# Optimization experiments

Hardware: AMD Instinct MI355X
Metric: run time of the kernel (lower is better)

## Reference

```python
import jax, jax.numpy as jnp
import numpy as np

D, K, N_NODES, E_DIM, H, L, HEADS, FF = 1024, 128, 200000, 384, 128, 2, 4, 128


def setup_inputs() -> dict:
    key = jax.random.key(0)
    ks = jax.random.split(key, 12)
    # regular graph: target node 0 has D neighbors (nodes 1..D); each neighbor n
    # has exactly K incoming edges, the first from tgt, the rest from random src != 0
    src = jax.random.randint(ks[0], (D, K), 1, N_NODES, dtype=jnp.int32)
    src = src.at[:, 0].set(0)
    dst = jnp.broadcast_to(jnp.arange(1, D + 1, dtype=jnp.int32)[:, None], (D, K))
    edge_index = jnp.stack([src.reshape(-1), dst.reshape(-1)])
    s = 0.05
    return {
        "tgt_x_index": jnp.zeros((1,), jnp.int32),
        "x": jax.random.normal(ks[1], (N_NODES, 64), jnp.float32),
        "edge_index": edge_index,
        "edge_attrs": jax.random.normal(ks[2], (D * K, E_DIM), jnp.float32),
        "first_token_marker": jax.random.normal(ks[3], (H,), jnp.float32),
        "proj_w": jax.random.normal(ks[4], (H, E_DIM), jnp.float32) * s,
        "proj_b": jnp.zeros((H,), jnp.float32),
        "attn_in_w": jax.random.normal(ks[5], (L, 3 * H, H), jnp.float32) * s,
        "attn_in_b": jnp.zeros((L, 3 * H), jnp.float32),
        "attn_out_w": jax.random.normal(ks[6], (L, H, H), jnp.float32) * s,
        "attn_out_b": jnp.zeros((L, H), jnp.float32),
        "ln1_g": jnp.ones((L, H), jnp.float32),
        "ln1_b": jnp.zeros((L, H), jnp.float32),
        "ff1_w": jax.random.normal(ks[7], (L, FF, H), jnp.float32) * s,
        "ff1_b": jnp.zeros((L, FF), jnp.float32),
        "ff2_w": jax.random.normal(ks[8], (L, H, FF), jnp.float32) * s,
        "ff2_b": jnp.zeros((L, H), jnp.float32),
        "ln2_g": jnp.ones((L, H), jnp.float32),
        "ln2_b": jnp.zeros((L, H), jnp.float32),
        "pred_w1": jax.random.normal(ks[9], (H, H), jnp.float32) * s,
        "pred_b1": jnp.zeros((H,), jnp.float32),
        "pred_w2": jax.random.normal(ks[10], (1, H), jnp.float32) * s,
        "pred_b2": jnp.zeros((1,), jnp.float32),
        "num_neighbors": D,
        "seq_len": K,
    }


def _ln(x, g, b):
    m = x.mean(-1, keepdims=True)
    v = ((x - m) ** 2).mean(-1, keepdims=True)
    return (x - m) * jax.lax.rsqrt(v + 1e-5) * g + b


def _forward(tgt_x_index, x, edge_index, edge_attrs, first_token_marker,
             proj_w, proj_b, attn_in_w, attn_in_b, attn_out_w, attn_out_b,
             ln1_g, ln1_b, ff1_w, ff1_b, ff2_w, ff2_b, ln2_g, ln2_b,
             pred_w1, pred_b1, pred_w2, pred_b2, num_neighbors, seq_len):
    tgt = tgt_x_index[0]
    src, dst = edge_index[0], edge_index[1]
    is_tgt = src == tgt
    # neighbors of target, in edge order (torch: edge_index[1][edge_index[0]==tgt])
    neigh_idx = jnp.nonzero(is_tgt, size=num_neighbors)[0]
    neigh_nodes = dst[neigh_idx]                       # [D]
    # fused ragged gather: map each edge to its neighbor slot, sort so that each
    # neighbor's edges are contiguous with the tgt->n edge first (stable sort
    # preserves original edge order within groups, matching boolean-mask gather)
    slot = jnp.full((x.shape[0],), num_neighbors, jnp.int32).at[neigh_nodes].set(
        jnp.arange(num_neighbors, dtype=jnp.int32))
    eslot = slot[dst]                                  # [E]
    sort_key = eslot.astype(jnp.int64) * 2 + jnp.where(is_tgt, 0, 1)
    order = jnp.argsort(sort_key)[: num_neighbors * seq_len]
    rows = edge_attrs[order].reshape(num_neighbors, seq_len, edge_attrs.shape[-1])
    hidden = proj_w.shape[0]
    hd = hidden // HEADS
    h = rows @ proj_w.T + proj_b                       # [D, K, H]
    h = h.at[:, 0, :].add(first_token_marker)          # first-token marker
    n_layers = attn_in_w.shape[0]
    for l in range(n_layers):
        qkv = h @ attn_in_w[l].T + attn_in_b[l]        # [D, K, 3H]
        q, k_, v = jnp.split(qkv, 3, axis=-1)
        q = q.reshape(num_neighbors, seq_len, HEADS, hd)
        k_ = k_.reshape(num_neighbors, seq_len, HEADS, hd)
        v = v.reshape(num_neighbors, seq_len, HEADS, hd)
        att = jax.nn.softmax(
            jnp.einsum('bqhd,bkhd->bhqk', q, k_) / jnp.sqrt(jnp.float32(hd)), axis=-1)
        o = jnp.einsum('bhqk,bkhd->bqhd', att, v).reshape(num_neighbors, seq_len, hidden)
        h = _ln(h + o @ attn_out_w[l].T + attn_out_b[l], ln1_g[l], ln1_b[l])
        f = jax.nn.relu(h @ ff1_w[l].T + ff1_b[l]) @ ff2_w[l].T + ff2_b[l]
        h = _ln(h + f, ln2_g[l], ln2_b[l])
    pooled = h.mean(axis=1)                            # mean over seq -> [D, H]
    final = pooled.mean(axis=0, keepdims=True)         # mean over neighbors -> [1, H]
    hmid = jax.nn.relu(final @ pred_w1.T + pred_b1)
    return jax.nn.sigmoid(hmid @ pred_w2.T + pred_b2)  # [1, 1]


def reference(tgt_x_index, x, edge_index, edge_attrs, first_token_marker,
              proj_w, proj_b, attn_in_w, attn_in_b, attn_out_w, attn_out_b,
              ln1_g, ln1_b, ff1_w, ff1_b, ff2_w, ff2_b, ln2_g, ln2_b,
              pred_w1, pred_b1, pred_w2, pred_b2, num_neighbors, seq_len):
    return _forward(tgt_x_index, x, edge_index, edge_attrs, first_token_marker,
                    proj_w, proj_b, attn_in_w, attn_in_b, attn_out_w, attn_out_b,
                    ln1_g, ln1_b, ff1_w, ff1_b, ff2_w, ff2_b, ln2_g, ln2_b,
                    pred_w1, pred_b1, pred_w2, pred_b2, num_neighbors, seq_len)
```

## Files before the change

### kernel.cpp

```cpp
#include <hip/hip_runtime.h>
#include <cstdint>
#include <cstddef>

#define D_N     1024
#define K_S     128
#define EDIM    384
#define HID     128
#define NHEAD   4
#define HDIM    32
#define FFD     128
#define NLAYER  2
#define ETOT    (D_N * K_S)
#define NNODES  200000
#define NBINS   (2 * D_N + 2)
#define NCH     1024
#define CHL     (ETOT / NCH)

#define OFF_ORDER 0u
#define OFF_KEY   0x080000u
#define OFF_SLOT  0x100000u
#define OFF_HIST  0x200000u
#define OFF_TOT   0xA02000u
#define OFF_WBF   0xA08000u
#define OFF_POOL  0xA80000u
#define WP_OFF 0
#define WI_OFF 49152
#define WO_OFF 147456
#define W1_OFF 180224
#define W2_OFF 212992
#define WTOT   245760

typedef __attribute__((ext_vector_type(8))) short  bf16x8;
typedef __attribute__((ext_vector_type(4))) short  short4v;
typedef __attribute__((ext_vector_type(4))) float  f32x4;

__device__ __forceinline__ short f2bf(float f) {
    union { float f; unsigned u; } v; v.f = f;
    unsigned r = v.u + 0x7fffu + ((v.u >> 16) & 1u);
    return (short)(r >> 16);
}
__device__ __forceinline__ int swz_off(int r, int byteInRow, int strideBytes) {
    return (r * strideBytes + byteInRow) ^ ((r & 7) << 4);
}

__global__ void init_cvt(int* __restrict__ slot, int* __restrict__ hist,
                         const float* __restrict__ p0, const float* __restrict__ p1,
                         const float* __restrict__ p2, const float* __restrict__ p3,
                         const float* __restrict__ p4, short* __restrict__ wbf)
{
    int idx = blockIdx.x * blockDim.x + threadIdx.x;
    int stride = gridDim.x * blockDim.x;
    for (int i = idx; i < NBINS * NCH; i += stride) hist[i] = 0;
    for (int i = idx; i < NNODES; i += stride) slot[i] = D_N;
    int i = idx * 8;
    if (i < WTOT) {
        const float* s;
        if      (i < WI_OFF) s = p0 + i;
        else if (i < WO_OFF) s = p1 + (i - WI_OFF);
        else if (i < W1_OFF) s = p2 + (i - WO_OFF);
        else if (i < W2_OFF) s = p3 + (i - W1_OFF);
        else                 s = p4 + (i - W2_OFF);
        float4 a = *(const float4*)s;
        float4 b = *(const float4*)(s + 4);
        bf16x8 o;
        o[0] = f2bf(a.x); o[1] = f2bf(a.y); o[2] = f2bf(a.z); o[3] = f2bf(a.w);
        o[4] = f2bf(b.x); o[5] = f2bf(b.y); o[6] = f2bf(b.z); o[7] = f2bf(b.w);
        *(bf16x8*)(wbf + i) = o;
    }
}

__global__ void find_neigh(const int* __restrict__ eidx,
                           const int* __restrict__ tgt_idx,
                           int* __restrict__ slot)
{
    __shared__ int wtot[16];
    __shared__ int wbase_s[16];
    __shared__ int neigh[D_N];
    const int tid  = threadIdx.x;
    const int lane = tid & 63;
    const int wv   = tid >> 6;
    const int tgt  = tgt_idx[0];
    const int* src = eidx;
    const int* dst = eidx + ETOT;
    const int epc  = ETOT / 1024;
    const int e0   = tid * epc;

    int c = 0;
    const int4* s4 = (const int4*)(src + e0);
    #pragma unroll 8
    for (int i = 0; i < epc / 4; ++i) {
        int4 v = s4[i];
        c += (v.x == tgt) + (v.y == tgt) + (v.z == tgt) + (v.w == tgt);
    }
    int incl = c;
    #pragma unroll
    for (int d = 1; d < 64; d <<= 1) {
        int t = __shfl_up(incl, d, 64);
        if (lane >= d) incl += t;
    }
    if (lane == 63) wtot[wv] = incl;
    __syncthreads();
    if (tid < 16) {
        int s = 0;
        for (int j = 0; j < tid; ++j) s += wtot[j];
        wbase_s[tid] = s;
    }
    __syncthreads();
    int r = wbase_s[wv] + incl - c;
    for (int e = e0; e < e0 + epc; ++e) {
        if (src[e] == tgt) { if (r < D_N) neigh[r] = dst[e]; ++r; }
    }
    __syncthreads();
    int total = wbase_s[15] + wtot[15];
    if (tid < total && tid < D_N) slot[neigh[tid]] = tid;
}

__global__ void compute_key(const int* __restrict__ eidx,
                            const int* __restrict__ tgt_idx,
                            const int* __restrict__ slot,
                            int* __restrict__ key)
{
    int e = blockIdx.x * 256 + threadIdx.x;
    if (e >= ETOT) return;
    int tgt = tgt_idx[0];
    key[e] = slot[eidx[ETOT + e]] * 2 + ((eidx[e] != tgt) ? 1 : 0);
}

__global__ void hist_build(const int* __restrict__ key, int* __restrict__ hist)
{
    const int c = blockIdx.x * 256 + threadIdx.x;
    if (c >= NCH) return;
    const int4* kp = (const int4*)(key + c * CHL);
    int cur = -1, run = 0;
    for (int i = 0; i < CHL / 4; ++i) {
        int4 k4 = kp[i];
        #pragma unroll
        for (int j = 0; j < 4; ++j) {
            int k = (j == 0) ? k4.x : (j == 1) ? k4.y : (j == 2) ? k4.z : k4.w;
            if (k == cur) { ++run; }
            else {
                if (run) hist[cur * NCH + c] += run;
                cur = k; run = 1;
            }
        }
    }
    if (run) hist[cur * NCH + c] += run;
}

__global__ void scan_pass1(const int* __restrict__ hist, int* __restrict__ tot)
{
    int b = blockIdx.x * 256 + threadIdx.x;
    if (b >= NBINS) return;
    const int4* h = (const int4*)(hist + b * NCH);
    int s = 0;
    #pragma unroll 4
    for (int c = 0; c < NCH / 4; ++c) { int4 v = h[c]; s += v.x + v.y + v.z + v.w; }
    tot[b] = s;
}

#define SCN 2176
__global__ void scan_pass2(int* __restrict__ tot)
{
    __shared__ int A[SCN];
    __shared__ int B[SCN];
    const int tid = threadIdx.x;
    for (int i = tid; i < SCN; i += 1024) A[i] = (i < NBINS) ? tot[i] : 0;
    __syncthreads();
    int* cur = A; int* nxt = B;
    for (int s = 1; s < SCN; s <<= 1) {
        for (int i = tid; i < SCN; i += 1024) nxt[i] = (i >= s) ? cur[i] + cur[i - s] : cur[i];
        __syncthreads();
        int* t = cur; cur = nxt; nxt = t;
    }
    for (int i = tid; i < NBINS; i += 1024) tot[i] = (i == 0) ? 0 : cur[i - 1];
}

__global__ void scan_pass3(int* __restrict__ hist, const int* __restrict__ base)
{
    const int wvg  = (blockIdx.x * blockDim.x + threadIdx.x) >> 6;
    const int lane = threadIdx.x & 63;
    if (wvg >= NBINS) return;
    int* h = hist + wvg * NCH + lane * 16;
    int4 a0 = ((int4*)h)[0], a1 = ((int4*)h)[1], a2 = ((int4*)h)[2], a3 = ((int4*)h)[3];
    int ls = a0.x + a0.y + a0.z + a0.w + a1.x + a1.y + a1.z + a1.w
           + a2.x + a2.y + a2.z + a2.w + a3.x + a3.y + a3.z + a3.w;
    int incl = ls;
    #pragma unroll
    for (int d = 1; d < 64; d <<= 1) {
        int t = __shfl_up(incl, d, 64);
        if (lane >= d) incl += t;
    }
    int run = base[wvg] + incl - ls;
    int4 o;
    o.x = run; run += a0.x; o.y = run; run += a0.y;
    o.z = run; run += a0.z; o.w = run; run += a0.w; ((int4*)h)[0] = o;
    o.x = run; run += a1.x; o.y = run; run += a1.y;
    o.z = run; run += a1.z; o.w = run; run += a1.w; ((int4*)h)[1] = o;
    o.x = run; run += a2.x; o.y = run; run += a2.y;
    o.z = run; run += a2.z; o.w = run; run += a2.w; ((int4*)h)[2] = o;
    o.x = run; run += a3.x; o.y = run; run += a3.y;
    o.z = run; run += a3.z; o.w = run; run += a3.w; ((int4*)h)[3] = o;
}

__global__ void scatter_order(const int* __restrict__ key,
                              int* __restrict__ hist,
                              int* __restrict__ order)
{
    const int c = blockIdx.x * 256 + threadIdx.x;
    if (c >= NCH) return;
    const int e0 = c * CHL;
    const int4* kp = (const int4*)(key + e0);
    int cur = -1, pos = 0;
    for (int i = 0; i < CHL / 4; ++i) {
        int4 k4 = kp[i];
        #pragma unroll
        for (int j = 0; j < 4; ++j) {
            int k = (j == 0) ? k4.x : (j == 1) ? k4.y : (j == 2) ? k4.z : k4.w;
            if (k != cur) {
                if (cur >= 0) hist[cur * NCH + c] = pos;
                cur = k;
                pos = hist[k * NCH + c];
            }
            if (pos >= 0 && pos < ETOT) order[pos] = e0 + i * 4 + j;
            ++pos;
        }
    }
    if (cur >= 0) hist[cur * NCH + c] = pos;
}

template<int CF, int KC, typename GetB>
__device__ __forceinline__ void gemm1(f32x4 (&acc)[CF],
    const char* aB, int aRow0, int aStride, int aColOff, int l15, int g, GetB getB)
{
    #pragma unroll
    for (int kc = 0; kc < KC; ++kc) {
        bf16x8 a = *(const bf16x8*)(aB +
            swz_off(aRow0 + l15, aColOff + kc * 64 + g * 16, aStride));
        #pragma unroll
        for (int cf = 0; cf < CF; ++cf)
            acc[cf] = __builtin_amdgcn_mfma_f32_16x16x32_bf16(a, getB(cf, kc), acc[cf], 0, 0, 0);
    }
}

template<int ROWB>
__device__ __forceinline__ void stage_w(const char* __restrict__ gsrc, char* ldst,
                                        int nbytes, int tid)
{
    #pragma unroll 4
    for (int u = tid * 16; u < nbytes; u += 512 * 16) {
        int row = u / ROWB;
        int in  = u - row * ROWB;
        *(bf16x8*)(ldst + swz_off(row, in, ROWB)) = *(const bf16x8*)(gsrc + u);
    }
}

template<int DROWB, int SROWB>
__device__ __forceinline__ void stage_sl(const char* __restrict__ gsrc, char* ldst,
                                         int nbytes, int tid)
{
    #pragma unroll 4
    for (int u = tid * 16; u < nbytes; u += 512 * 16) {
        int row = u / DROWB;
        int in  = u - row * DROWB;
        *(bf16x8*)(ldst + swz_off(row, in, DROWB)) =
            *(const bf16x8*)(gsrc + (size_t)row * SROWB + in);
    }
}

__device__ __forceinline__ void layer_norm1(f32x4 (&x)[8],
    const float* __restrict__ gg, const float* __restrict__ bb, int l15)
{
    float gv[8], bv[8];
    #pragma unroll
    for (int cf = 0; cf < 8; ++cf) { gv[cf] = gg[l15 + 16 * cf]; bv[cf] = bb[l15 + 16 * cf]; }
    #pragma unroll
    for (int rg = 0; rg < 4; ++rg) {
        float s = 0.f;
        #pragma unroll
        for (int cf = 0; cf < 8; ++cf) s += x[cf][rg];
        s += __shfl_xor(s, 1); s += __shfl_xor(s, 2);
        s += __shfl_xor(s, 4); s += __shfl_xor(s, 8);
        float mean = s * (1.f / 128.f);
        float v = 0.f;
        #pragma unroll
        for (int cf = 0; cf < 8; ++cf) { float d = x[cf][rg] - mean; v += d * d; }
        v += __shfl_xor(v, 1); v += __shfl_xor(v, 2);
        v += __shfl_xor(v, 4); v += __shfl_xor(v, 8);
        float rs = rsqrtf(v * (1.f / 128.f) + 1e-5f);
        #pragma unroll
        for (int cf = 0; cf < 8; ++cf)
            x[cf][rg] = (x[cf][rg] - mean) * rs * gv[cf] + bv[cf];
    }
}

__device__ __forceinline__ void write_hbf(const f32x4 (&x)[8], char* hbf_n,
                                          int l15, int g, int row0)
{
    #pragma unroll
    for (int cf = 0; cf < 8; ++cf)
        #pragma unroll
        for (int rg = 0; rg < 4; ++rg)
            *(short*)(hbf_n + swz_off(row0 + g * 4 + rg, (l15 + 16 * cf) * 2, 256)) =
                f2bf(x[cf][rg]);
}

__device__ __forceinline__ void attn_one(char* qb, const char* kb, const char* vb,
    const short* __restrict__ WOl, f32x4 (&hx)[8], int hd, int l15, int g, int row0)
{
    f32x4 sc[8];
    #pragma unroll
    for (int cf = 0; cf < 8; ++cf) sc[cf] = (f32x4){0.f, 0.f, 0.f, 0.f};
    gemm1<8, 1>(sc, qb, row0, 64, 0, l15, g,
        [&](int cf, int kc) {
            (void)kc;
            return *(const bf16x8*)(kb + swz_off(l15 + 16 * cf, g * 16, 64));
        });
    const float SC_ = 0.17677669529663687f;
    float inv_s[4];
    #pragma unroll
    for (int rg = 0; rg < 4; ++rg) {
        float mx = -1e30f;
        #pragma unroll
        for (int cf = 0; cf < 8; ++cf) {
            sc[cf][rg] *= SC_;
            mx = fmaxf(mx, sc[cf][rg]);
        }
        mx = fmaxf(mx, __shfl_xor(mx, 1)); mx = fmaxf(mx, __shfl_xor(mx, 2));
        mx = fmaxf(mx, __shfl_xor(mx, 4)); mx = fmaxf(mx, __shfl_xor(mx, 8));
        float sum = 0.f;
        #pragma unroll
        for (int cf = 0; cf < 8; ++cf) {
            float e = __expf(sc[cf][rg] - mx);
            sc[cf][rg] = e; sum += e;
        }
        sum += __shfl_xor(sum, 1); sum += __shfl_xor(sum, 2);
        sum += __shfl_xor(sum, 4); sum += __shfl_xor(sum, 8);
        inv_s[rg] = 1.f / sum;
    }
    f32x4 ov[2];
    ov[0] = (f32x4){0.f, 0.f, 0.f, 0.f};
    ov[1] = (f32x4){0.f, 0.f, 0.f, 0.f};
    #pragma unroll
    for (int cc = 0; cc < 4; ++cc) {
        #pragma unroll
        for (int q = 0; q < 2; ++q) {
            int cfi = 2 * cc + q;
            #pragma unroll
            for (int rg = 0; rg < 4; ++rg)
                *(short*)(qb + swz_off(row0 + g * 4 + rg, (l15 + 16 * q) * 2, 64)) =
                    f2bf(sc[cfi][rg] * inv_s[rg]);
        }
        gemm1<2, 1>(ov, qb, row0, 64, 0, l15, g,
            [&](int cf, int kc) {
                (void)kc;
                return *(const bf16x8*)(vb + swz_off(l15 + 16 * cf, cc * 64 + g * 16, 256));
            });
    }
    #pragma unroll
    for (int cf = 0; cf < 2; ++cf)
        #pragma unroll
        for (int rg = 0; rg < 4; ++rg)
            *(short*)(qb + swz_off(row0 + g * 4 + rg, (l15 + 16 * cf) * 2, 64)) =
                f2bf(ov[cf][rg]);
    gemm1<8, 1>(hx, qb, row0, 64, 0, l15, g,
        [&](int cf, int kc) {
            (void)kc;
            return *(const bf16x8*)(WOl +
                (size_t)(l15 + 16 * cf) * HID + hd * HDIM + g * 8);
        });
}

#define LDS_TOTAL 73728
__global__ __launch_bounds__(512, 2) void fused_mfma(
    const float* __restrict__ edge_attrs,
    const float* __restrict__ ftm,
    const short* __restrict__ wP, const float* __restrict__ projb,
    const short* __restrict__ wI, const float* __restrict__ aib,
    const short* __restrict__ wO, const float* __restrict__ aob,
    const float* __restrict__ l1g, const float* __restrict__ l1b,
    const short* __restrict__ w1, const float* __restrict__ f1b,
    const short* __restrict__ w2, const float* __restrict__ f2b,
    const float* __restrict__ l2g, const float* __restrict__ l2b,
    const int*   __restrict__ order,
    float*       __restrict__ pooled)
{
    __shared__ __align__(16) char sm[LDS_TOTAL];
    char* hbf  = sm;
    char* qkv  = sm + 32768;
    char* q_l  = qkv;
    char* k_l  = qkv + 8192;
    char* vT   = qkv + 16384;
    char* wb   = sm + 57344;
    char* wbB  = qkv + 8192;
    char* ebuf = qkv;
    char* fbuf = q_l;

    const int tid  = threadIdx.x;
    const int w    = tid >> 6;
    const int l    = tid & 63;
    const int l15  = l & 15;
    const int g    = l >> 4;
    const int row0 = 16 * w;
    const int b    = blockIdx.x;

    f32x4 hx[8];

    {
        #pragma unroll
        for (int cf = 0; cf < 8; ++cf) {
            float bs = projb[l15 + 16 * cf];
            hx[cf] = (f32x4){bs, bs, bs, bs};
        }
        const int prow = row0 + (l >> 2);
        const int rowIdx = order[b * K_S + prow];
        const float* arow = edge_attrs + (size_t)rowIdx * EDIM;
        const int doff = (l & 3) * 16;

        for (int ch = 0; ch < 6; ++ch) {
            stage_sl<128, 768>((const char*)wP + ch * 128, wb, 16384, tid);
            #pragma unroll
            for (int j = 0; j < 2; ++j) {
                float4 v0 = *(const float4*)(arow + ch * 64 + doff + j * 8);
                float4 v1 = *(const float4*)(arow + ch * 64 + doff + j * 8 + 4);
                bf16x8 pk;
                pk[0] = f2bf(v0.x); pk[1] = f2bf(v0.y); pk[2] = f2bf(v0.z); pk[3] = f2bf(v0.w);
                pk[4] = f2bf(v1.x); pk[5] = f2bf(v1.y); pk[6] = f2bf(v1.z); pk[7] = f2bf(v1.w);
                *(bf16x8*)(ebuf + swz_off(prow, (doff + j * 8) * 2, 128)) = pk;
            }
            __syncthreads();
            gemm1<8, 2>(hx, ebuf, row0, 128, 0, l15, g,
                [&](int cf, int kc) {
                    return *(const bf16x8*)(wb + swz_off(l15 + 16 * cf, kc * 64 + g * 16, 128));
                });
            __syncthreads();
        }
        if (w == 0 && g == 0) {
            #pragma unroll
            for (int cf = 0; cf < 8; ++cf) hx[cf][0] += ftm[l15 + 16 * cf];
        }
        write_hbf(hx, hbf, l15, g, row0);
        stage_w<256>((const char*)wI, wb, 8192, tid);
        stage_w<256>((const char*)(wI + (size_t)HID * HID), wb + 8192, 8192, tid);
        __syncthreads();
    }

    for (int ly = 0; ly < NLAYER; ++ly) {
        const short* WIl = wI + (size_t)ly * 3 * HID * HID;
        const float* bI  = aib + ly * 3 * HID;
        const short* WOl = wO + (size_t)ly * HID * HID;
        const float* bO  = aob + ly * HID;
        const short* W1l = w1 + (size_t)ly * FFD * HID;
        const float* b1  = f1b + ly * FFD;
        const short* W2l = w2 + (size_t)ly * HID * FFD;
        const float* b2v = f2b + ly * HID;

        #pragma unroll
        for (int cf = 0; cf < 8; ++cf) {
            float bs = bO[l15 + 16 * cf];
            #pragma unroll
            for (int rg = 0; rg < 4; ++rg) hx[cf][rg] += bs;
        }

        for (int hd = 0; hd < NHEAD; ++hd) {
            f32x4 acc[6];
            #pragma unroll
            for (int cf = 0; cf < 6; ++cf) {
                float bs = bI[(cf >> 1) * HID + hd * HDIM + l15 + 16 * (cf & 1)];
                acc[cf] = (f32x4){bs, bs, bs, bs};
            }
            gemm1<6, 4>(acc, hbf, row0, 256, 0, l15, g,
                [&](int cf, int kc) {
                    if (cf < 2)
                        return *(const bf16x8*)(wb +
                            swz_off(l15 + 16 * cf, kc * 64 + g * 16, 256));
                    else if (cf < 4)
                        return *(const bf16x8*)(wb + 8192 +
                            swz_off(l15 + 16 * (cf - 2), kc * 64 + g * 16, 256));
                    else
                        return *(const bf16x8*)(WIl +
                            (size_t)(2 * HID + hd * HDIM + l15 + 16 * (cf - 4)) * HID +
                            kc * 32 + g * 8);
                });
            #pragma unroll
            for (int cf = 0; cf < 2; ++cf) {
                int dcol = (l15 + 16 * cf) * 2;
                #pragma unroll
                for (int rg = 0; rg < 4; ++rg) {
                    int row = row0 + g * 4 + rg;
                    *(short*)(q_l + swz_off(row, dcol, 64)) = f2bf(acc[cf][rg]);
                    *(short*)(k_l + swz_off(row, dcol, 64)) = f2bf(acc[2 + cf][rg]);
                }
                short4v pv;
                pv[0] = f2bf(acc[4 + cf][0]); pv[1] = f2bf(acc[4 + cf][1]);
                pv[2] = f2bf(acc[4 + cf][2]); pv[3] = f2bf(acc[4 + cf][3]);
                *(short4v*)(vT + swz_off(l15 + 16 * cf, (row0 + g * 4) * 2, 256)) = pv;
            }
            __syncthreads();

            if (hd < NHEAD - 1) {
                stage_w<256>((const char*)(WIl + (size_t)((hd + 1) * HDIM) * HID),
                             wb, 8192, tid);
                stage_w<256>((const char*)(WIl + (size_t)(HID + (hd + 1) * HDIM) * HID),
                             wb + 8192, 8192, tid);
            } else {
                stage_w<256>((const char*)W1l, wb, 8192, tid);
                stage_sl<64, 256>((const char*)W2l, wb + 8192, 8192, tid);
            }
            attn_one(q_l, k_l, vT, WOl, hx, hd, l15, g, row0);
            __syncthreads();
        }

        layer_norm1(hx, l1g + ly * HID, l1b + ly * HID, l15);
        write_hbf(hx, hbf, l15, g, row0);

        f32x4 yy[8];
        #pragma unroll
        for (int cf = 0; cf < 8; ++cf) {
            float bs = b2v[l15 + 16 * cf];
            yy[cf] = (f32x4){bs, bs, bs, bs};
        }
        #pragma unroll
        for (int qq = 0; qq < 4; ++qq) {
            char* bw = (qq & 1) ? wbB : wb;
            f32x4 fq[2];
            #pragma unroll
            for (int cf = 0; cf < 2; ++cf) {
                float bs = b1[qq * 32 + l15 + 16 * cf];
                fq[cf] = (f32x4){bs, bs, bs, bs};
            }
            gemm1<2, 4>(fq, hbf, row0, 256, 0, l15, g,
                [&](int cf, int kc) {
                    return *(const bf16x8*)(bw + swz_off(l15 + 16 * cf, kc * 64 + g * 16, 256));
                });
            if (qq < 3) {
                char* nb = (qq & 1) ? wb : wbB;
                stage_w<256>((const char*)(W1l + (size_t)((qq + 1) * 32) * HID),
                             nb, 8192, tid);
                stage_sl<64, 256>((const char*)W2l + (qq + 1) * 64, nb + 8192, 8192, tid);
            } else if (ly + 1 < NLAYER) {
                const short* WIn = wI + (size_t)(ly + 1) * 3 * HID * HID;
                stage_w<256>((const char*)WIn, wb, 8192, tid);
                stage_w<256>((const char*)(WIn + (size_t)HID * HID), wb + 8192, 8192, tid);
            }
            #pragma unroll
            for (int cf = 0; cf < 2; ++cf)
                #pragma unroll
                for (int rg = 0; rg < 4; ++rg)
                    *(short*)(fbuf + swz_off(row0 + g * 4 + rg, (l15 + 16 * cf) * 2, 64)) =
                        f2bf(fmaxf(fq[cf][rg], 0.f));
            gemm1<8, 1>(yy, fbuf, row0, 64, 0, l15, g,
                [&](int cf, int kc) {
                    (void)kc;
                    return *(const bf16x8*)(bw + 8192 + swz_off(l15 + 16 * cf, g * 16, 64));
                });
            __syncthreads();
        }
        #pragma unroll
        for (int cf = 0; cf < 8; ++cf) yy[cf] += hx[cf];
        layer_norm1(yy, l2g + ly * HID, l2b + ly * HID, l15);
        #pragma unroll
        for (int cf = 0; cf < 8; ++cf) hx[cf] = yy[cf];
        write_hbf(hx, hbf, l15, g, row0);
    }

    float* pool_s = (float*)qkv;
    #pragma unroll
    for (int cf = 0; cf < 8; ++cf) {
        float s = hx[cf][0] + hx[cf][1] + hx[cf][2] + hx[cf][3];
        s += __shfl_xor(s, 16); s += __shfl_xor(s, 32);
        if (g == 0) pool_s[w * 128 + l15 + 16 * cf] = s;
    }
    __syncthreads();
    if (tid < 128) {
        float s = 0.f;
        #pragma unroll
        for (int ww = 0; ww < 8; ++ww) s += pool_s[ww * 128 + tid];
        pooled[b * HID + tid] = s * (1.f / 128.f);
    }
}

__global__ void final_pred(const float* __restrict__ pooled,
                           const float* __restrict__ w1, const float* __restrict__ b1,
                           const float* __restrict__ w2, const float* __restrict__ b2,
                           float* __restrict__ out)
{
    __shared__ float part[4][HID];
    __shared__ float fin[HID];
    __shared__ float hm[HID];
    const int tid = threadIdx.x;
    const int f = tid & 127, q = tid >> 7;
    float s = 0.f;
    for (int bb = q * 256; bb < (q + 1) * 256; ++bb) s += pooled[bb * HID + f];
    part[q][f] = s;
    __syncthreads();
    if (tid < HID) {
        fin[tid] = (part[0][tid] + part[1][tid] + part[2][tid] + part[3][tid])
                   * (1.f / (float)D_N);
    }
    __syncthreads();
    if (tid < HID) {
        float a = b1[tid];
        for (int k = 0; k < HID; ++k) a += fin[k] * w1[tid * HID + k];
        hm[tid] = fmaxf(a, 0.f) * w2[tid];
    }
    __syncthreads();
    if (tid == 0) {
        float z = 0.f;
        for (int j = 0; j < HID; ++j) z += hm[j];
        z += b2[0];
        out[0] = 1.f / (1.f + __expf(-z));
    }
}

extern "C" void kernel_launch(void* const* d_in, const int* in_sizes, int n_in,
                              void* d_out, int out_size, void* d_ws, size_t ws_size,
                              hipStream_t stream)
{
    (void)in_sizes; (void)n_in; (void)out_size; (void)ws_size;

    const int*   tgt   = (const int*)  d_in[0];
    const int*   eidx  = (const int*)  d_in[2];
    const float* eattr = (const float*)d_in[3];
    const float* ftm   = (const float*)d_in[4];
    const float* projw = (const float*)d_in[5];
    const float* projb = (const float*)d_in[6];
    const float* aiw   = (const float*)d_in[7];
    const float* aib   = (const float*)d_in[8];
    const float* aow   = (const float*)d_in[9];
    const float* aob   = (const float*)d_in[10];
    const float* l1g   = (const float*)d_in[11];
    const float* l1b   = (const float*)d_in[12];
    const float* f1w   = (const float*)d_in[13];
    const float* f1b   = (const float*)d_in[14];
    const float* f2w   = (const float*)d_in[15];
    const float* f2b   = (const float*)d_in[16];
    const float* l2g   = (const float*)d_in[17];
    const float* l2b   = (const float*)d_in[18];
    const float* pw1   = (const float*)d_in[19];
    const float* pb1   = (const float*)d_in[20];
    const float* pw2   = (const float*)d_in[21];
    const float* pb2   = (const float*)d_in[22];

    char* ws = (char*)d_ws;
    int*   order  = (int*)  (ws + OFF_ORDER);
    int*   key    = (int*)  (ws + OFF_KEY);
    int*   slot   = (int*)  (ws + OFF_SLOT);
    int*   hist   = (int*)  (ws + OFF_HIST);
    int*   tot    = (int*)  (ws + OFF_TOT);
    float* pooled = (float*)(ws + OFF_POOL);
    short* wbf    = (short*)(ws + OFF_WBF);

    init_cvt     <<<dim3(2048), dim3(256),  0, stream>>>(slot, hist,
                                                         projw, aiw, aow, f1w, f2w, wbf);
    find_neigh   <<<dim3(1),    dim3(1024), 0, stream>>>(eidx, tgt, slot);
    compute_key  <<<dim3(512),  dim3(256),  0, stream>>>(eidx, tgt, slot, key);
    hist_build   <<<dim3(4),    dim3(256),  0, stream>>>(key, hist);
    scan_pass1   <<<dim3(9),    dim3(256),  0, stream>>>(hist, tot);
    scan_pass2   <<<dim3(1),    dim3(1024), 0, stream>>>(tot);
    scan_pass3   <<<dim3(513),  dim3(256),  0, stream>>>(hist, tot);
    scatter_order<<<dim3(4),    dim3(256),  0, stream>>>(key, hist, order);

    fused_mfma<<<dim3(D_N), dim3(512), 0, stream>>>(
        eattr, ftm,
        wbf + WP_OFF, projb,
        wbf + WI_OFF, aib,
        wbf + WO_OFF, aob,
        l1g, l1b,
        wbf + W1_OFF, f1b,
        wbf + W2_OFF, f2b,
        l2g, l2b,
        order, pooled);

    final_pred<<<dim3(1), dim3(512), 0, stream>>>(pooled, pw1, pb1, pw2, pb2, (float*)d_out);
}
```

Baseline: 511.5 us.

## Process two neighbor sequences per 1024-thread block sharing staged weights with double buffering

Each block now handles two neighbor sequences with 1024 threads, so weight tiles staged into LDS are shared by both sequences and staged half as often per sequence. The projection and QKV weight staging uses two ping-pong buffers so the next chunk loads while the current one is consumed, and the V weights come from LDS instead of global memory. In exchange LDS use grows to 160KB per block, which allows only one block per CU, and each barrier now spans 16 waves.

After: 566.4 us. 10.7% more time.

```diff
diff --git a/kernel.cpp b/kernel.cpp
--- a/kernel.cpp
+++ b/kernel.cpp
@@ -246,8 +246,8 @@
 __device__ __forceinline__ void stage_w(const char* __restrict__ gsrc, char* ldst,
                                         int nbytes, int tid)
 {
-    #pragma unroll 4
-    for (int u = tid * 16; u < nbytes; u += 512 * 16) {
+    #pragma unroll 2
+    for (int u = tid * 16; u < nbytes; u += 1024 * 16) {
         int row = u / ROWB;
         int in  = u - row * ROWB;
         *(bf16x8*)(ldst + swz_off(row, in, ROWB)) = *(const bf16x8*)(gsrc + u);
@@ -258,8 +258,8 @@
 __device__ __forceinline__ void stage_sl(const char* __restrict__ gsrc, char* ldst,
                                          int nbytes, int tid)
 {
-    #pragma unroll 4
-    for (int u = tid * 16; u < nbytes; u += 512 * 16) {
+    #pragma unroll 2
+    for (int u = tid * 16; u < nbytes; u += 1024 * 16) {
         int row = u / DROWB;
         int in  = u - row * DROWB;
         *(bf16x8*)(ldst + swz_off(row, in, DROWB)) =
@@ -370,8 +370,8 @@
         });
 }
 
-#define LDS_TOTAL 73728
-__global__ __launch_bounds__(512, 2) void fused_mfma(
+#define LDS_TOTAL 163840
+__global__ __launch_bounds__(1024) void fused_mfma(
     const float* __restrict__ edge_attrs,
     const float* __restrict__ ftm,
     const short* __restrict__ wP, const float* __restrict__ projb,
@@ -385,23 +385,23 @@
     float*       __restrict__ pooled)
 {
     __shared__ __align__(16) char sm[LDS_TOTAL];
-    char* hbf  = sm;
-    char* qkv  = sm + 32768;
-    char* q_l  = qkv;
-    char* k_l  = qkv + 8192;
-    char* vT   = qkv + 16384;
-    char* wb   = sm + 57344;
-    char* wbB  = qkv + 8192;
-    char* ebuf = qkv;
+    const int tid = threadIdx.x;
+    const int w   = tid >> 6;
+    const int nb  = w >> 3;
+    const int l   = tid & 63;
+    const int l15 = l & 15;
+    const int g   = l >> 4;
+    const int row0 = (w & 7) * 16;
+    const int b   = blockIdx.x;
+
+    char* hbf  = sm + nb * 32768;
+    char* q_l  = sm + 65536 + nb * 16384;
+    char* k_l  = q_l + 8192;
+    char* vT   = sm + 98304 + nb * 8192;
+    char* ebuf = q_l;
     char* fbuf = q_l;
-
-    const int tid  = threadIdx.x;
-    const int w    = tid >> 6;
-    const int l    = tid & 63;
-    const int l15  = l & 15;
-    const int g    = l >> 4;
-    const int row0 = 16 * w;
-    const int b    = blockIdx.x;
+    char* wb0  = sm + 114688;
+    char* wb1  = sm + 139264;
 
     f32x4 hx[8];
 
@@ -412,12 +412,15 @@
             hx[cf] = (f32x4){bs, bs, bs, bs};
         }
         const int prow = row0 + (l >> 2);
-        const int rowIdx = order[b * K_S + prow];
+        const int rowIdx = order[(2 * b + nb) * K_S + prow];
         const float* arow = edge_attrs + (size_t)rowIdx * EDIM;
         const int doff = (l & 3) * 16;
 
+        stage_sl<128, 768>((const char*)wP, wb0, 16384, tid);
+        __syncthreads();
+
         for (int ch = 0; ch < 6; ++ch) {
-            stage_sl<128, 768>((const char*)wP + ch * 128, wb, 16384, tid);
+            char* cw = (ch & 1) ? wb1 : wb0;
             #pragma unroll
             for (int j = 0; j < 2; ++j) {
                 float4 v0 = *(const float4*)(arow + ch * 64 + doff + j * 8);
@@ -427,21 +430,26 @@
                 pk[4] = f2bf(v1.x); pk[5] = f2bf(v1.y); pk[6] = f2bf(v1.z); pk[7] = f2bf(v1.w);
                 *(bf16x8*)(ebuf + swz_off(prow, (doff + j * 8) * 2, 128)) = pk;
             }
+            if (ch < 5) {
+                stage_sl<128, 768>((const char*)wP + (ch + 1) * 128,
+                                   (ch & 1) ? wb0 : wb1, 16384, tid);
+            } else {
+                stage_w<256>((const char*)wI, wb0, 8192, tid);
+                stage_w<256>((const char*)(wI + (size_t)HID * HID), wb0 + 8192, 8192, tid);
+                stage_w<256>((const char*)(wI + (size_t)(2 * HID) * HID), wb0 + 16384, 8192, tid);
+            }
             __syncthreads();
             gemm1<8, 2>(hx, ebuf, row0, 128, 0, l15, g,
                 [&](int cf, int kc) {
-                    return *(const bf16x8*)(wb + swz_off(l15 + 16 * cf, kc * 64 + g * 16, 128));
+                    return *(const bf16x8*)(cw + swz_off(l15 + 16 * cf, kc * 64 + g * 16, 128));
                 });
             __syncthreads();
         }
-        if (w == 0 && g == 0) {
+        if ((w & 7) == 0 && g == 0) {
             #pragma unroll
             for (int cf = 0; cf < 8; ++cf) hx[cf][0] += ftm[l15 + 16 * cf];
         }
         write_hbf(hx, hbf, l15, g, row0);
-        stage_w<256>((const char*)wI, wb, 8192, tid);
-        stage_w<256>((const char*)(wI + (size_t)HID * HID), wb + 8192, 8192, tid);
-        __syncthreads();
     }
 
     for (int ly = 0; ly < NLAYER; ++ly) {
@@ -462,6 +470,7 @@
         }
 
         for (int hd = 0; hd < NHEAD; ++hd) {
+            char* cw = (hd & 1) ? wb1 : wb0;
             f32x4 acc[6];
             #pragma unroll
             for (int cf = 0; cf < 6; ++cf) {
@@ -470,16 +479,8 @@
             }
             gemm1<6, 4>(acc, hbf, row0, 256, 0, l15, g,
                 [&](int cf, int kc) {
-                    if (cf < 2)
-                        return *(const bf16x8*)(wb +
-                            swz_off(l15 + 16 * cf, kc * 64 + g * 16, 256));
-                    else if (cf < 4)
-                        return *(const bf16x8*)(wb + 8192 +
-                            swz_off(l15 + 16 * (cf - 2), kc * 64 + g * 16, 256));
-                    else
-                        return *(const bf16x8*)(WIl +
-                            (size_t)(2 * HID + hd * HDIM + l15 + 16 * (cf - 4)) * HID +
-                            kc * 32 + g * 8);
+                    return *(const bf16x8*)(cw + (cf >> 1) * 8192 +
+                        swz_off(l15 + 16 * (cf & 1), kc * 64 + g * 16, 256));
                 });
             #pragma unroll
             for (int cf = 0; cf < 2; ++cf) {
@@ -497,14 +498,17 @@
             }
             __syncthreads();
 
+            char* nw = (hd & 1) ? wb0 : wb1;
             if (hd < NHEAD - 1) {
                 stage_w<256>((const char*)(WIl + (size_t)((hd + 1) * HDIM) * HID),
-                             wb, 8192, tid);
+                             nw, 8192, tid);
                 stage_w<256>((const char*)(WIl + (size_t)(HID + (hd + 1) * HDIM) * HID),
-                             wb + 8192, 8192, tid);
+                             nw + 8192, 8192, tid);
+                stage_w<256>((const char*)(WIl + (size_t)(2 * HID + (hd + 1) * HDIM) * HID),
+                             nw + 16384, 8192, tid);
             } else {
-                stage_w<256>((const char*)W1l, wb, 8192, tid);
-                stage_sl<64, 256>((const char*)W2l, wb + 8192, 8192, tid);
+                stage_w<256>((const char*)W1l, nw, 8192, tid);
+                stage_sl<64, 256>((const char*)W2l, nw + 8192, 8192, tid);
             }
             attn_one(q_l, k_l, vT, WOl, hx, hd, l15, g, row0);
             __syncthreads();
@@ -521,7 +525,7 @@
         }
         #pragma unroll
         for (int qq = 0; qq < 4; ++qq) {
-            char* bw = (qq & 1) ? wbB : wb;
+            char* bw = (qq & 1) ? wb1 : wb0;
             f32x4 fq[2];
             #pragma unroll
             for (int cf = 0; cf < 2; ++cf) {
@@ -532,15 +536,16 @@
                 [&](int cf, int kc) {
                     return *(const bf16x8*)(bw + swz_off(l15 + 16 * cf, kc * 64 + g * 16, 256));
                 });
+            char* nw = (qq & 1) ? wb0 : wb1;
             if (qq < 3) {
-                char* nb = (qq & 1) ? wb : wbB;
                 stage_w<256>((const char*)(W1l + (size_t)((qq + 1) * 32) * HID),
-                             nb, 8192, tid);
-                stage_sl<64, 256>((const char*)W2l + (qq + 1) * 64, nb + 8192, 8192, tid);
+                             nw, 8192, tid);
+                stage_sl<64, 256>((const char*)W2l + (qq + 1) * 64, nw + 8192, 8192, tid);
             } else if (ly + 1 < NLAYER) {
                 const short* WIn = wI + (size_t)(ly + 1) * 3 * HID * HID;
-                stage_w<256>((const char*)WIn, wb, 8192, tid);
-                stage_w<256>((const char*)(WIn + (size_t)HID * HID), wb + 8192, 8192, tid);
+                stage_w<256>((const char*)WIn, wb0, 8192, tid);
+                stage_w<256>((const char*)(WIn + (size_t)HID * HID), wb0 + 8192, 8192, tid);
+                stage_w<256>((const char*)(WIn + (size_t)(2 * HID) * HID), wb0 + 16384, 8192, tid);
             }
             #pragma unroll
             for (int cf = 0; cf < 2; ++cf)
@@ -563,19 +568,22 @@
         write_hbf(hx, hbf, l15, g, row0);
     }
 
-    float* pool_s = (float*)qkv;
+    float* pool_n = (float*)(wb0 + nb * 4096);
     #pragma unroll
     for (int cf = 0; cf < 8; ++cf) {
         float s = hx[cf][0] + hx[cf][1] + hx[cf][2] + hx[cf][3];
         s += __shfl_xor(s, 16); s += __shfl_xor(s, 32);
-        if (g == 0) pool_s[w * 128 + l15 + 16 * cf] = s;
-    }
-    __syncthreads();
-    if (tid < 128) {
+        if (g == 0) pool_n[(w & 7) * 128 + l15 + 16 * cf] = s;
+    }
+    __syncthreads();
+    if (tid < 256) {
+        const int f  = tid & 127;
+        const int nn = tid >> 7;
+        const float* ps = (const float*)(wb0 + nn * 4096);
         float s = 0.f;
         #pragma unroll
-        for (int ww = 0; ww < 8; ++ww) s += pool_s[ww * 128 + tid];
-        pooled[b * HID + tid] = s * (1.f / 128.f);
+        for (int ww = 0; ww < 8; ++ww) s += ps[ww * 128 + f];
+        pooled[(2 * b + nn) * HID + f] = s * (1.f / 128.f);
     }
 }
 
@@ -660,7 +668,7 @@
     scan_pass3   <<<dim3(513),  dim3(256),  0, stream>>>(hist, tot);
     scatter_order<<<dim3(4),    dim3(256),  0, stream>>>(key, hist, order);
 
-    fused_mfma<<<dim3(D_N), dim3(512), 0, stream>>>(
+    fused_mfma<<<dim3(D_N / 2), dim3(1024), 0, stream>>>(
         eattr, ftm,
         wbf + WP_OFF, projb,
         wbf + WI_OFF, aib,
```

## Shrink LDS footprint by reading K and W2 weights from global, double-buffer projection

Applied to the files above, without the earlier changes.

Cuts the shared-memory allocation from 72KB to 64KB. To fit, the K-projection weights and the FF2 weights are no longer staged in LDS and are read directly from global memory (L2) inside the MFMA loops. The input-projection weight chunks are double-buffered in the not-yet-used hidden-state region, so staging the next chunk overlaps compute and one barrier per chunk is removed. The trade-off is more global-memory latency in the inner GEMMs, in exchange for less LDS pressure, possibly better occupancy, and less sync in the projection phase.

Measured after the change: 597.3 us. 16.8% more time.

```diff
diff --git a/kernel.cpp b/kernel.cpp
--- a/kernel.cpp
+++ b/kernel.cpp
@@ -370,7 +370,7 @@
         });
 }
 
-#define LDS_TOTAL 73728
+#define LDS_TOTAL 65536
 __global__ __launch_bounds__(512, 2) void fused_mfma(
     const float* __restrict__ edge_attrs,
     const float* __restrict__ ftm,
@@ -386,14 +386,13 @@
 {
     __shared__ __align__(16) char sm[LDS_TOTAL];
     char* hbf  = sm;
-    char* qkv  = sm + 32768;
-    char* q_l  = qkv;
-    char* k_l  = qkv + 8192;
-    char* vT   = qkv + 16384;
+    char* q_l  = sm + 32768;
+    char* k_l  = sm + 40960;
+    char* vT   = sm + 49152;
     char* wb   = sm + 57344;
-    char* wbB  = qkv + 8192;
-    char* ebuf = qkv;
-    char* fbuf = q_l;
+    char* pw0  = hbf;
+    char* pw1  = hbf + 16384;
+    char* ebuf = q_l;
 
     const int tid  = threadIdx.x;
     const int w    = tid >> 6;
@@ -416,8 +415,12 @@
         const float* arow = edge_attrs + (size_t)rowIdx * EDIM;
         const int doff = (l & 3) * 16;
 
+        stage_sl<128, 768>((const char*)wP, pw0, 16384, tid);
+        stage_sl<128, 768>((const char*)wP + 128, pw1, 16384, tid);
+        __syncthreads();
+
         for (int ch = 0; ch < 6; ++ch) {
-            stage_sl<128, 768>((const char*)wP + ch * 128, wb, 16384, tid);
+            char* cw = (ch & 1) ? pw1 : pw0;
             #pragma unroll
             for (int j = 0; j < 2; ++j) {
                 float4 v0 = *(const float4*)(arow + ch * 64 + doff + j * 8);
@@ -425,23 +428,25 @@
                 bf16x8 pk;
                 pk[0] = f2bf(v0.x); pk[1] = f2bf(v0.y); pk[2] = f2bf(v0.z); pk[3] = f2bf(v0.w);
                 pk[4] = f2bf(v1.x); pk[5] = f2bf(v1.y); pk[6] = f2bf(v1.z); pk[7] = f2bf(v1.w);
-                *(bf16x8*)(ebuf + swz_off(prow, (doff + j * 8) * 2, 128)) = pk;
+                *(bf16x8*)(ebuf + swz_off(prow, doff * 2 + j * 16, 128)) = pk;
             }
-            __syncthreads();
             gemm1<8, 2>(hx, ebuf, row0, 128, 0, l15, g,
                 [&](int cf, int kc) {
-                    return *(const bf16x8*)(wb + swz_off(l15 + 16 * cf, kc * 64 + g * 16, 128));
+                    return *(const bf16x8*)(cw +
+                        swz_off(l15 + 16 * cf, kc * 64 + g * 16, 128));
                 });
             __syncthreads();
-        }
+            if (ch + 2 < 6)
+                stage_sl<128, 768>((const char*)wP + (ch + 2) * 128, cw, 16384, tid);
+            else if (ch + 2 == 6)
+                stage_w<256>((const char*)wI, wb, 8192, tid);
+        }
+        __syncthreads();
         if (w == 0 && g == 0) {
             #pragma unroll
             for (int cf = 0; cf < 8; ++cf) hx[cf][0] += ftm[l15 + 16 * cf];
         }
         write_hbf(hx, hbf, l15, g, row0);
-        stage_w<256>((const char*)wI, wb, 8192, tid);
-        stage_w<256>((const char*)(wI + (size_t)HID * HID), wb + 8192, 8192, tid);
-        __syncthreads();
     }
 
     for (int ly = 0; ly < NLAYER; ++ly) {
@@ -473,13 +478,10 @@
                     if (cf < 2)
                         return *(const bf16x8*)(wb +
                             swz_off(l15 + 16 * cf, kc * 64 + g * 16, 256));
-                    else if (cf < 4)
-                        return *(const bf16x8*)(wb + 8192 +
-                            swz_off(l15 + 16 * (cf - 2), kc * 64 + g * 16, 256));
-                    else
-                        return *(const bf16x8*)(WIl +
-                            (size_t)(2 * HID + hd * HDIM + l15 + 16 * (cf - 4)) * HID +
-                            kc * 32 + g * 8);
+                    int sec = cf >> 1;
+                    return *(const bf16x8*)(WIl +
+                        (size_t)(sec * HID + hd * HDIM + l15 + 16 * (cf & 1)) * HID +
+                        kc * 32 + g * 8);
                 });
             #pragma unroll
             for (int cf = 0; cf < 2; ++cf) {
@@ -497,15 +499,11 @@
             }
             __syncthreads();
 
-            if (hd < NHEAD - 1) {
+            if (hd < NHEAD - 1)
                 stage_w<256>((const char*)(WIl + (size_t)((hd + 1) * HDIM) * HID),
                              wb, 8192, tid);
-                stage_w<256>((const char*)(WIl + (size_t)(HID + (hd + 1) * HDIM) * HID),
-                             wb + 8192, 8192, tid);
-            } else {
+            else
                 stage_w<256>((const char*)W1l, wb, 8192, tid);
-                stage_sl<64, 256>((const char*)W2l, wb + 8192, 8192, tid);
-            }
             attn_one(q_l, k_l, vT, WOl, hx, hd, l15, g, row0);
             __syncthreads();
         }
@@ -521,7 +519,7 @@
         }
         #pragma unroll
         for (int qq = 0; qq < 4; ++qq) {
-            char* bw = (qq & 1) ? wbB : wb;
+            char* bw = (qq == 0) ? wb : (qq == 1) ? k_l : (qq == 2) ? vT : k_l;
             f32x4 fq[2];
             #pragma unroll
             for (int cf = 0; cf < 2; ++cf) {
@@ -530,28 +528,29 @@
             }
             gemm1<2, 4>(fq, hbf, row0, 256, 0, l15, g,
                 [&](int cf, int kc) {
-                    return *(const bf16x8*)(bw + swz_off(l15 + 16 * cf, kc * 64 + g * 16, 256));
+                    return *(const bf16x8*)(bw +
+                        swz_off(l15 + 16 * cf, kc * 64 + g * 16, 256));
                 });
-            if (qq < 3) {
-                char* nb = (qq & 1) ? wb : wbB;
-                stage_w<256>((const char*)(W1l + (size_t)((qq + 1) * 32) * HID),
-                             nb, 8192, tid);
-                stage_sl<64, 256>((const char*)W2l + (qq + 1) * 64, nb + 8192, 8192, tid);
-            } else if (ly + 1 < NLAYER) {
-                const short* WIn = wI + (size_t)(ly + 1) * 3 * HID * HID;
-                stage_w<256>((const char*)WIn, wb, 8192, tid);
-                stage_w<256>((const char*)(WIn + (size_t)HID * HID), wb + 8192, 8192, tid);
-            }
+            if (qq == 0)
+                stage_w<256>((const char*)(W1l + (size_t)32 * HID), k_l, 8192, tid);
+            else if (qq == 1)
+                stage_w<256>((const char*)(W1l + (size_t)64 * HID), vT, 8192, tid);
+            else if (qq == 2)
+                stage_w<256>((const char*)(W1l + (size_t)96 * HID), k_l, 8192, tid);
+            else if (ly + 1 < NLAYER)
+                stage_w<256>((const char*)(wI + (size_t)(ly + 1) * 3 * HID * HID),
+                             wb, 8192, tid);
             #pragma unroll
             for (int cf = 0; cf < 2; ++cf)
                 #pragma unroll
                 for (int rg = 0; rg < 4; ++rg)
-                    *(short*)(fbuf + swz_off(row0 + g * 4 + rg, (l15 + 16 * cf) * 2, 64)) =
+                    *(short*)(q_l + swz_off(row0 + g * 4 + rg, (l15 + 16 * cf) * 2, 64)) =
                         f2bf(fmaxf(fq[cf][rg], 0.f));
-            gemm1<8, 1>(yy, fbuf, row0, 64, 0, l15, g,
+            gemm1<8, 1>(yy, q_l, row0, 64, 0, l15, g,
                 [&](int cf, int kc) {
                     (void)kc;
-                    return *(const bf16x8*)(bw + 8192 + swz_off(l15 + 16 * cf, g * 16, 64));
+                    return *(const bf16x8*)(W2l +
+                        (size_t)(l15 + 16 * cf) * FFD + qq * 32 + g * 8);
                 });
             __syncthreads();
         }
@@ -563,7 +562,7 @@
         write_hbf(hx, hbf, l15, g, row0);
     }
 
-    float* pool_s = (float*)qkv;
+    float* pool_s = (float*)q_l;
     #pragma unroll
     for (int cf = 0; cf < 8; ++cf) {
         float s = hx[cf][0] + hx[cf][1] + hx[cf][2] + hx[cf][3];
```
